# Performance work log

Hardware: AMD Instinct MI355X
Metric: run time of the kernel (lower is better)

The kernel has to match this reference:

```python
import jax, jax.numpy as jnp
import numpy as np

IN_DIM = 1024
OUT_DIM = 128
N = 8192


def setup_inputs() -> dict:
    key = jax.random.key(0)
    ks = jax.random.split(key, 7)
    s = 1.0 / np.sqrt(IN_DIM)
    return {
        "z": jax.random.normal(ks[0], (N, IN_DIM), dtype=jnp.float32),
        "Wq": jax.random.normal(ks[1], (IN_DIM, OUT_DIM), dtype=jnp.float32) * s,
        "bq": jax.random.normal(ks[2], (OUT_DIM,), dtype=jnp.float32) * 0.01,
        "Wk": jax.random.normal(ks[3], (IN_DIM, OUT_DIM), dtype=jnp.float32) * s,
        "bk": jax.random.normal(ks[4], (OUT_DIM,), dtype=jnp.float32) * 0.01,
        "Wv": jax.random.normal(ks[5], (IN_DIM, OUT_DIM), dtype=jnp.float32) * s,
        "bv": jax.random.normal(ks[6], (OUT_DIM,), dtype=jnp.float32) * 0.01,
    }


def reference(z, Wq, bq, Wk, bk, Wv, bv):
    # QKV projections: [N, in_dim] @ [in_dim, out_dim] + bias -> [N, out_dim]
    q = z @ Wq + bq
    k = z @ Wk + bk
    v = z @ Wv + bv
    dh = q.shape[-1]
    # Scores [N, N], scaled by sqrt(dh); softmax over last axis (torch 2-D default)
    scores = (q @ k.T) * (1.0 / jnp.sqrt(jnp.asarray(dh, q.dtype)))
    A = jax.nn.softmax(scores, axis=-1)
    return A @ v
```

## Files before the change

kernel.cpp:

```cpp
#include <hip/hip_runtime.h>


#define N_TOK   8192
#define D_IN    1024
#define D_HEAD  128
#define QSCALE  (0.08838834764831845f * 1.4426950408889634f)
#define SPLIT   8
#define QB      128
#define KVB     64
#define NIT     ((N_TOK / SPLIT) / KVB)

typedef _Float16 half8 __attribute__((ext_vector_type(8)));
typedef _Float16 half4 __attribute__((ext_vector_type(4)));
typedef float f32x4 __attribute__((ext_vector_type(4)));

__global__ void prep_wt(const float* __restrict__ Wq, const float* __restrict__ Wk,
                        const float* __restrict__ Wv, _Float16* __restrict__ Wt) {
    __shared__ float T[32][129];
    const int mat = blockIdx.y;
    const int k0 = blockIdx.x * 32;
    const int t = threadIdx.x;
    const float* W = (mat == 0) ? Wq : (mat == 1) ? Wk : Wv;

    const int krow = t >> 3, nc0 = (t & 7) * 16;
#pragma unroll
    for (int i = 0; i < 4; i++) {
        float4 f = reinterpret_cast<const float4*>(
            W + (size_t)(k0 + krow) * D_HEAD + nc0)[i];
        T[krow][nc0 + i * 4 + 0] = f.x;
        T[krow][nc0 + i * 4 + 1] = f.y;
        T[krow][nc0 + i * 4 + 2] = f.z;
        T[krow][nc0 + i * 4 + 3] = f.w;
    }
    __syncthreads();

    const int n = t >> 1, kh = (t & 1) * 16;
    half8 h0, h1;
#pragma unroll
    for (int j = 0; j < 8; j++) {
        float v0 = T[kh + j][n];
        float v1 = T[kh + 8 + j][n];
        if (mat == 0) { v0 *= QSCALE; v1 *= QSCALE; }
        h0[j] = (_Float16)v0;
        h1[j] = (_Float16)v1;
    }
    _Float16* dst = Wt + (size_t)mat * 131072 + (size_t)n * D_IN + k0 + kh;
    reinterpret_cast<half8*>(dst)[0] = h0;
    reinterpret_cast<half8*>(dst)[1] = h1;
}

__launch_bounds__(256)
__global__ void qkv_gemm(const float* __restrict__ z, const _Float16* __restrict__ Wt,
                         const float* __restrict__ bq, const float* __restrict__ bk,
                         const float* __restrict__ bv,
                         _Float16* __restrict__ Qs, _Float16* __restrict__ Kh,
                         _Float16* __restrict__ Vt) {
    __shared__ __align__(16) char lds[32768];
    char* Ab = lds;
    char* Bb = lds + 16384;

    const int mat = blockIdx.y;
    const int m0 = blockIdx.x * 128;
    const int t = threadIdx.x;
    const int lane = t & 63, w = t >> 6;
    const int l15 = lane & 15, g = lane >> 4;
    const int wm = w >> 1, wn = w & 1;
    const _Float16* Wm = Wt + (size_t)mat * 131072;

    const int srow = t >> 1, sh = t & 1;
    int aw[4], bw[4];
#pragma unroll
    for (int i = 0; i < 4; i++) {
        int u = ((sh * 4 + i) ^ (srow & 7)) << 4;
        aw[i] = srow * 128 + u;
        bw[i] = srow * 128 + u;
    }
    int ru[2];
#pragma unroll
    for (int ct = 0; ct < 2; ct++) ru[ct] = ((ct * 4 + g) ^ (l15 & 7)) << 4;

    f32x4 acc[4][4] = {};

    const float4* zg = reinterpret_cast<const float4*>(
        z + (size_t)(m0 + srow) * D_IN + sh * 32);
    const half8* wg = reinterpret_cast<const half8*>(
        Wm + (size_t)srow * D_IN + sh * 32);

    float4 af[8];
    half8 bf[4];
#pragma unroll
    for (int i = 0; i < 8; i++) af[i] = zg[i];
#pragma unroll
    for (int i = 0; i < 4; i++) bf[i] = wg[i];

    for (int it = 0; it < 16; ++it) {
        __syncthreads();
#pragma unroll
        for (int j = 0; j < 4; j++) {
            half8 h;
            float4 lo = af[2 * j], hi = af[2 * j + 1];
            h[0]=(_Float16)lo.x; h[1]=(_Float16)lo.y; h[2]=(_Float16)lo.z; h[3]=(_Float16)lo.w;
            h[4]=(_Float16)hi.x; h[5]=(_Float16)hi.y; h[6]=(_Float16)hi.z; h[7]=(_Float16)hi.w;
            *reinterpret_cast<half8*>(Ab + aw[j]) = h;
            *reinterpret_cast<half8*>(Bb + bw[j]) = bf[j];
        }
        __syncthreads();

        if (it < 15) {
            zg += 16;
            wg += 8;
#pragma unroll
            for (int i = 0; i < 8; i++) af[i] = zg[i];
#pragma unroll
            for (int i = 0; i < 4; i++) bf[i] = wg[i];
        }

        __builtin_amdgcn_s_setprio(1);
#pragma unroll
        for (int ct = 0; ct < 2; ct++) {
            half8 afr[4], bfr[4];
#pragma unroll
            for (int m16 = 0; m16 < 4; m16++)
                afr[m16] = *reinterpret_cast<half8*>(
                    Ab + (wm * 64 + m16 * 16 + l15) * 128 + ru[ct]);
#pragma unroll
            for (int n16 = 0; n16 < 4; n16++)
                bfr[n16] = *reinterpret_cast<half8*>(
                    Bb + (wn * 64 + n16 * 16 + l15) * 128 + ru[ct]);
#pragma unroll
            for (int m16 = 0; m16 < 4; m16++)
#pragma unroll
                for (int n16 = 0; n16 < 4; n16++)
                    acc[m16][n16] = __builtin_amdgcn_mfma_f32_16x16x32_f16(
                        afr[m16], bfr[n16], acc[m16][n16], 0, 0, 0);
        }
        __builtin_amdgcn_s_setprio(0);
    }

    const float* bias = (mat == 0) ? bq : (mat == 1) ? bk : bv;
    if (mat < 2) {
        _Float16* dst = (mat == 0) ? Qs : Kh;
#pragma unroll
        for (int n16 = 0; n16 < 4; n16++) {
            int n = wn * 64 + n16 * 16 + l15;
            float b = bias[n];
            if (mat == 0) b *= QSCALE;
#pragma unroll
            for (int m16 = 0; m16 < 4; m16++)
#pragma unroll
                for (int r = 0; r < 4; r++) {
                    int m = m0 + wm * 64 + m16 * 16 + g * 4 + r;
                    dst[(size_t)m * D_HEAD + n] = (_Float16)(acc[m16][n16][r] + b);
                }
        }
    } else {
#pragma unroll
        for (int n16 = 0; n16 < 4; n16++) {
            int n = wn * 64 + n16 * 16 + l15;
            float b = bias[n];
#pragma unroll
            for (int m16 = 0; m16 < 4; m16++) {
                half4 pk;
#pragma unroll
                for (int r = 0; r < 4; r++) pk[r] = (_Float16)(acc[m16][n16][r] + b);
                int m = m0 + wm * 64 + m16 * 16 + g * 4;
                *reinterpret_cast<half4*>(&Vt[(size_t)n * N_TOK + m]) = pk;
            }
        }
    }
}

__launch_bounds__(256, 2)
__global__ void attn(const _Float16* __restrict__ Qs, const _Float16* __restrict__ Kh,
                     const _Float16* __restrict__ Vt,
                     _Float16* __restrict__ Opart, float* __restrict__ lpart) {
    __shared__ __align__(16) char lds[49152];
    char* Kb = lds;
    char* Vb = lds + 16384;
    char* Pb = lds + 32768;

    const int t = threadIdx.x;
    const int lane = t & 63, w = t >> 6;
    const int l15 = lane & 15, g = lane >> 4;
    const int q0 = blockIdx.x * QB;
    const int sp = blockIdx.y;
    const int kvA = sp * (N_TOK / SPLIT);

    half8 qa[2][4];
#pragma unroll
    for (int r16 = 0; r16 < 2; r16++)
#pragma unroll
        for (int ct = 0; ct < 4; ct++)
            qa[r16][ct] = *reinterpret_cast<const half8*>(
                Qs + (size_t)(q0 + w * 32 + r16 * 16 + l15) * D_HEAD + ct * 32 + g * 8);

    const int krow = t >> 2, kseg = t & 3;
    const int vd = t >> 1, vh = t & 1;
    int kw[4], vw[4];
#pragma unroll
    for (int i = 0; i < 4; i++) {
        kw[i] = krow * 256 + (((kseg * 4 + i) ^ (krow & 7)) << 4);
        vw[i] = vd * 128 + (((vh * 4 + i) ^ (vd & 7)) << 4);
    }
    int kru[4], vru[2];
#pragma unroll
    for (int ct = 0; ct < 4; ct++) kru[ct] = ((ct * 4 + g) ^ (l15 & 7)) << 4;
#pragma unroll
    for (int s2 = 0; s2 < 2; s2++) vru[s2] = ((s2 * 4 + g) ^ (l15 & 7)) << 4;
    char* Pw = Pb + w * 4096;
    const int phi = l15 >> 3, plo = (l15 & 7) * 2;
    int px[4];
#pragma unroll
    for (int r = 0; r < 4; r++) px[r] = (g * 4 + r) & 7;

    f32x4 o[2][8] = {};
    float lsum[2][4] = {};

    const _Float16* kg = Kh + (size_t)(kvA + krow) * D_HEAD + kseg * 32;
    const _Float16* vg = Vt + (size_t)vd * N_TOK + kvA + vh * 32;
    half8 kr[4], vr[4];
#pragma unroll
    for (int i = 0; i < 4; i++) {
        kr[i] = reinterpret_cast<const half8*>(kg)[i];
        vr[i] = reinterpret_cast<const half8*>(vg)[i];
    }

    for (int it = 0; it < NIT; ++it) {
        __syncthreads();
#pragma unroll
        for (int i = 0; i < 4; i++) {
            *reinterpret_cast<half8*>(Kb + kw[i]) = kr[i];
            *reinterpret_cast<half8*>(Vb + vw[i]) = vr[i];
        }
        __syncthreads();

        if (it + 1 < NIT) {
            kg += (size_t)KVB * D_HEAD;
            vg += KVB;
#pragma unroll
            for (int i = 0; i < 4; i++) {
                kr[i] = reinterpret_cast<const half8*>(kg)[i];
                vr[i] = reinterpret_cast<const half8*>(vg)[i];
            }
        }

        f32x4 sf[2][4] = {};
        __builtin_amdgcn_s_setprio(1);
#pragma unroll
        for (int kt = 0; kt < 4; kt++) {
#pragma unroll
            for (int ct = 0; ct < 4; ct++) {
                half8 kf = *reinterpret_cast<half8*>(Kb + kt * 4096 + l15 * 256 + kru[ct]);
#pragma unroll
                for (int r16 = 0; r16 < 2; r16++)
                    sf[r16][kt] = __builtin_amdgcn_mfma_f32_16x16x32_f16(
                        qa[r16][ct], kf, sf[r16][kt], 0, 0, 0);
            }
        }
        __builtin_amdgcn_s_setprio(0);

#pragma unroll
        for (int r16 = 0; r16 < 2; r16++)
#pragma unroll
            for (int kt = 0; kt < 4; kt++)
#pragma unroll
                for (int r = 0; r < 4; r++) {
                    float p = __builtin_amdgcn_exp2f(sf[r16][kt][r]);
                    lsum[r16][r] += p;
                    *reinterpret_cast<_Float16*>(
                        Pw + r16 * 2048 + (g * 4 + r) * 128 +
                        (((kt * 2 + phi) ^ px[r]) << 4) + plo) = (_Float16)p;
                }

        __builtin_amdgcn_s_setprio(1);
#pragma unroll
        for (int s2 = 0; s2 < 2; s2++) {
            half8 pa[2];
#pragma unroll
            for (int r16 = 0; r16 < 2; r16++)
                pa[r16] = *reinterpret_cast<half8*>(Pw + r16 * 2048 + l15 * 128 + vru[s2]);
#pragma unroll
            for (int dt = 0; dt < 8; dt++) {
                half8 vf = *reinterpret_cast<half8*>(Vb + dt * 2048 + l15 * 128 + vru[s2]);
#pragma unroll
                for (int r16 = 0; r16 < 2; r16++)
                    o[r16][dt] = __builtin_amdgcn_mfma_f32_16x16x32_f16(
                        pa[r16], vf, o[r16][dt], 0, 0, 0);
            }
        }
        __builtin_amdgcn_s_setprio(0);
    }

#pragma unroll
    for (int r16 = 0; r16 < 2; r16++)
#pragma unroll
        for (int r = 0; r < 4; r++) {
            float v = lsum[r16][r];
            v += __shfl_xor(v, 1, 64);
            v += __shfl_xor(v, 2, 64);
            v += __shfl_xor(v, 4, 64);
            v += __shfl_xor(v, 8, 64);
            lsum[r16][r] = v;
        }

    _Float16* Op = Opart + (size_t)sp * N_TOK * D_HEAD;
#pragma unroll
    for (int r16 = 0; r16 < 2; r16++)
#pragma unroll
        for (int dt = 0; dt < 8; dt++)
#pragma unroll
            for (int r = 0; r < 4; r++)
                Op[(size_t)(q0 + w * 32 + r16 * 16 + g * 4 + r) * D_HEAD + dt * 16 + l15] =
                    (_Float16)o[r16][dt][r];
    if (l15 == 0) {
#pragma unroll
        for (int r16 = 0; r16 < 2; r16++)
#pragma unroll
            for (int r = 0; r < 4; r++)
                lpart[sp * N_TOK + q0 + w * 32 + r16 * 16 + g * 4 + r] = lsum[r16][r];
    }
}

__global__ void combine(const _Float16* __restrict__ Opart, const float* __restrict__ lpart,
                        float* __restrict__ out) {
    int i = blockIdx.x * 256 + threadIdx.x;
    int base = i * 8;
    int m = base >> 7;
    float acc[8] = {};
    float den = 0.f;
#pragma unroll
    for (int s = 0; s < SPLIT; s++) {
        half8 h = *reinterpret_cast<const half8*>(
            Opart + (size_t)s * N_TOK * D_HEAD + base);
#pragma unroll
        for (int j = 0; j < 8; j++) acc[j] += (float)h[j];
        den += lpart[s * N_TOK + m];
    }
    float inv = 1.f / den;
    float4 o0, o1;
    o0.x = acc[0]*inv; o0.y = acc[1]*inv; o0.z = acc[2]*inv; o0.w = acc[3]*inv;
    o1.x = acc[4]*inv; o1.y = acc[5]*inv; o1.z = acc[6]*inv; o1.w = acc[7]*inv;
    reinterpret_cast<float4*>(out + base)[0] = o0;
    reinterpret_cast<float4*>(out + base)[1] = o1;
}

extern "C" void kernel_launch(void* const* d_in, const int* in_sizes, int n_in,
                              void* d_out, int out_size, void* d_ws, size_t ws_size,
                              hipStream_t stream) {
    const float* z  = (const float*)d_in[0];
    const float* Wq = (const float*)d_in[1];
    const float* bq = (const float*)d_in[2];
    const float* Wk = (const float*)d_in[3];
    const float* bk = (const float*)d_in[4];
    const float* Wv = (const float*)d_in[5];
    const float* bv = (const float*)d_in[6];
    float* out = (float*)d_out;

    char* ws = (char*)d_ws;
    _Float16* Wt = (_Float16*)(ws);
    _Float16* Qs = (_Float16*)(ws + 786432);
    _Float16* Kh = (_Float16*)(ws + 786432 + 2097152);
    _Float16* Vt = (_Float16*)(ws + 786432 + 2 * 2097152);
    _Float16* Opart = (_Float16*)(ws + 786432 + 3 * 2097152);
    float* lpart = (float*)(ws + 786432 + 3 * 2097152 +
                            (size_t)SPLIT * N_TOK * D_HEAD * 2);

    prep_wt<<<dim3(32, 3), 256, 0, stream>>>(Wq, Wk, Wv, Wt);
    qkv_gemm<<<dim3(64, 3), 256, 0, stream>>>(z, Wt, bq, bk, bv, Qs, Kh, Vt);
    attn<<<dim3(N_TOK / QB, SPLIT), 256, 0, stream>>>(Qs, Kh, Vt, Opart, lpart);
    combine<<<512, 256, 0, stream>>>(Opart, lpart, out);
}
```

Measured before the change: 159.7 us.

## Double-buffer K/V in LDS and pass P through registers via shuffles

```diff
diff --git a/kernel.cpp b/kernel.cpp
--- a/kernel.cpp
+++ b/kernel.cpp
@@ -13,6 +13,13 @@
 typedef _Float16 half8 __attribute__((ext_vector_type(8)));
 typedef _Float16 half4 __attribute__((ext_vector_type(4)));
 typedef float f32x4 __attribute__((ext_vector_type(4)));
+
+static __device__ __forceinline__ int pkrtz(float a, float b) {
+    auto h = __builtin_amdgcn_cvt_pkrtz(a, b);
+    return __builtin_bit_cast(int, h);
+}
+
+union I4H8 { int i[4]; half8 h; };
 
 __global__ void prep_wt(const float* __restrict__ Wq, const float* __restrict__ Wk,
                         const float* __restrict__ Wv, _Float16* __restrict__ Wt) {
@@ -174,10 +181,7 @@
 __global__ void attn(const _Float16* __restrict__ Qs, const _Float16* __restrict__ Kh,
                      const _Float16* __restrict__ Vt,
                      _Float16* __restrict__ Opart, float* __restrict__ lpart) {
-    __shared__ __align__(16) char lds[49152];
-    char* Kb = lds;
-    char* Vb = lds + 16384;
-    char* Pb = lds + 32768;
+    __shared__ __align__(16) char lds[65536];
 
     const int t = threadIdx.x;
     const int lane = t & 63, w = t >> 6;
@@ -188,11 +192,11 @@
 
     half8 qa[2][4];
 #pragma unroll
-    for (int r16 = 0; r16 < 2; r16++)
+    for (int qg = 0; qg < 2; qg++)
 #pragma unroll
         for (int ct = 0; ct < 4; ct++)
-            qa[r16][ct] = *reinterpret_cast<const half8*>(
-                Qs + (size_t)(q0 + w * 32 + r16 * 16 + l15) * D_HEAD + ct * 32 + g * 8);
+            qa[qg][ct] = *reinterpret_cast<const half8*>(
+                Qs + (size_t)(q0 + w * 32 + qg * 16 + l15) * D_HEAD + ct * 32 + g * 8);
 
     const int krow = t >> 2, kseg = t & 3;
     const int vd = t >> 1, vh = t & 1;
@@ -206,15 +210,14 @@
 #pragma unroll
     for (int ct = 0; ct < 4; ct++) kru[ct] = ((ct * 4 + g) ^ (l15 & 7)) << 4;
 #pragma unroll
-    for (int s2 = 0; s2 < 2; s2++) vru[s2] = ((s2 * 4 + g) ^ (l15 & 7)) << 4;
-    char* Pw = Pb + w * 4096;
-    const int phi = l15 >> 3, plo = (l15 & 7) * 2;
-    int px[4];
-#pragma unroll
-    for (int r = 0; r < 4; r++) px[r] = (g * 4 + r) & 7;
+    for (int ks = 0; ks < 2; ks++) vru[ks] = ((ks * 4 + g) ^ (l15 & 7)) << 4;
+
+    const int s0 = l15 + 32 * (g & 1);
+    const int s1 = s0 + 16;
+    const bool hi_t = (g & 2) != 0;
 
     f32x4 o[2][8] = {};
-    float lsum[2][4] = {};
+    float lsum[2] = {0.f, 0.f};
 
     const _Float16* kg = Kh + (size_t)(kvA + krow) * D_HEAD + kseg * 32;
     const _Float16* vg = Vt + (size_t)vd * N_TOK + kvA + vh * 32;
@@ -224,17 +227,49 @@
         kr[i] = reinterpret_cast<const half8*>(kg)[i];
         vr[i] = reinterpret_cast<const half8*>(vg)[i];
     }
+#pragma unroll
+    for (int i = 0; i < 4; i++) {
+        *reinterpret_cast<half8*>(lds + kw[i])         = kr[i];
+        *reinterpret_cast<half8*>(lds + 16384 + vw[i]) = vr[i];
+    }
+    kg += (size_t)KVB * D_HEAD;
+    vg += KVB;
+#pragma unroll
+    for (int i = 0; i < 4; i++) {
+        kr[i] = reinterpret_cast<const half8*>(kg)[i];
+        vr[i] = reinterpret_cast<const half8*>(vg)[i];
+    }
+    __syncthreads();
 
     for (int it = 0; it < NIT; ++it) {
-        __syncthreads();
-#pragma unroll
-        for (int i = 0; i < 4; i++) {
-            *reinterpret_cast<half8*>(Kb + kw[i]) = kr[i];
-            *reinterpret_cast<half8*>(Vb + vw[i]) = vr[i];
-        }
-        __syncthreads();
+        char* Kb = lds + (it & 1) * 32768;
+        char* Vb = Kb + 16384;
+        char* Kn = lds + ((it & 1) ^ 1) * 32768;
+        char* Vn = Kn + 16384;
+
+        f32x4 sf[2][4] = {};
+        __builtin_amdgcn_s_setprio(1);
+#pragma unroll
+        for (int kt = 0; kt < 4; kt++) {
+#pragma unroll
+            for (int ct = 0; ct < 4; ct++) {
+                half8 kf = *reinterpret_cast<half8*>(Kb + kt * 4096 + l15 * 256 + kru[ct]);
+#pragma unroll
+                for (int qg = 0; qg < 2; qg++)
+                    sf[qg][kt] = __builtin_amdgcn_mfma_f32_16x16x32_f16(
+                        kf, qa[qg][ct], sf[qg][kt], 0, 0, 0);
+            }
+        }
+        __builtin_amdgcn_s_setprio(0);
 
         if (it + 1 < NIT) {
+#pragma unroll
+            for (int i = 0; i < 4; i++) {
+                *reinterpret_cast<half8*>(Kn + kw[i]) = kr[i];
+                *reinterpret_cast<half8*>(Vn + vw[i]) = vr[i];
+            }
+        }
+        if (it + 2 < NIT) {
             kg += (size_t)KVB * D_HEAD;
             vg += KVB;
 #pragma unroll
@@ -244,80 +279,79 @@
             }
         }
 
-        f32x4 sf[2][4] = {};
+        int pk[2][4][2];
+#pragma unroll
+        for (int qg = 0; qg < 2; qg++)
+#pragma unroll
+            for (int kt = 0; kt < 4; kt++) {
+                float e0 = __builtin_amdgcn_exp2f(sf[qg][kt][0]);
+                float e1 = __builtin_amdgcn_exp2f(sf[qg][kt][1]);
+                float e2 = __builtin_amdgcn_exp2f(sf[qg][kt][2]);
+                float e3 = __builtin_amdgcn_exp2f(sf[qg][kt][3]);
+                lsum[qg] += (e0 + e1) + (e2 + e3);
+                pk[qg][kt][0] = pkrtz(e0, e1);
+                pk[qg][kt][1] = pkrtz(e2, e3);
+            }
+
         __builtin_amdgcn_s_setprio(1);
 #pragma unroll
-        for (int kt = 0; kt < 4; kt++) {
-#pragma unroll
-            for (int ct = 0; ct < 4; ct++) {
-                half8 kf = *reinterpret_cast<half8*>(Kb + kt * 4096 + l15 * 256 + kru[ct]);
-#pragma unroll
-                for (int r16 = 0; r16 < 2; r16++)
-                    sf[r16][kt] = __builtin_amdgcn_mfma_f32_16x16x32_f16(
-                        qa[r16][ct], kf, sf[r16][kt], 0, 0, 0);
+        for (int ks = 0; ks < 2; ks++) {
+            half8 pa[2];
+#pragma unroll
+            for (int qg = 0; qg < 2; qg++) {
+                int a0 = __shfl(pk[qg][2 * ks][0],     s0);
+                int b0 = __shfl(pk[qg][2 * ks + 1][0], s0);
+                int a1 = __shfl(pk[qg][2 * ks][1],     s0);
+                int b1 = __shfl(pk[qg][2 * ks + 1][1], s0);
+                int a2 = __shfl(pk[qg][2 * ks][0],     s1);
+                int b2 = __shfl(pk[qg][2 * ks + 1][0], s1);
+                int a3 = __shfl(pk[qg][2 * ks][1],     s1);
+                int b3 = __shfl(pk[qg][2 * ks + 1][1], s1);
+                I4H8 u;
+                u.i[0] = hi_t ? b0 : a0;
+                u.i[1] = hi_t ? b1 : a1;
+                u.i[2] = hi_t ? b2 : a2;
+                u.i[3] = hi_t ? b3 : a3;
+                pa[qg] = u.h;
+            }
+#pragma unroll
+            for (int dt = 0; dt < 8; dt++) {
+                half8 vf = *reinterpret_cast<half8*>(Vb + dt * 2048 + l15 * 128 + vru[ks]);
+#pragma unroll
+                for (int qg = 0; qg < 2; qg++)
+                    o[qg][dt] = __builtin_amdgcn_mfma_f32_16x16x32_f16(
+                        vf, pa[qg], o[qg][dt], 0, 0, 0);
             }
         }
         __builtin_amdgcn_s_setprio(0);
 
-#pragma unroll
-        for (int r16 = 0; r16 < 2; r16++)
-#pragma unroll
-            for (int kt = 0; kt < 4; kt++)
-#pragma unroll
-                for (int r = 0; r < 4; r++) {
-                    float p = __builtin_amdgcn_exp2f(sf[r16][kt][r]);
-                    lsum[r16][r] += p;
-                    *reinterpret_cast<_Float16*>(
-                        Pw + r16 * 2048 + (g * 4 + r) * 128 +
-                        (((kt * 2 + phi) ^ px[r]) << 4) + plo) = (_Float16)p;
-                }
-
-        __builtin_amdgcn_s_setprio(1);
-#pragma unroll
-        for (int s2 = 0; s2 < 2; s2++) {
-            half8 pa[2];
-#pragma unroll
-            for (int r16 = 0; r16 < 2; r16++)
-                pa[r16] = *reinterpret_cast<half8*>(Pw + r16 * 2048 + l15 * 128 + vru[s2]);
-#pragma unroll
-            for (int dt = 0; dt < 8; dt++) {
-                half8 vf = *reinterpret_cast<half8*>(Vb + dt * 2048 + l15 * 128 + vru[s2]);
-#pragma unroll
-                for (int r16 = 0; r16 < 2; r16++)
-                    o[r16][dt] = __builtin_amdgcn_mfma_f32_16x16x32_f16(
-                        pa[r16], vf, o[r16][dt], 0, 0, 0);
-            }
-        }
-        __builtin_amdgcn_s_setprio(0);
-    }
-
-#pragma unroll
-    for (int r16 = 0; r16 < 2; r16++)
-#pragma unroll
-        for (int r = 0; r < 4; r++) {
-            float v = lsum[r16][r];
-            v += __shfl_xor(v, 1, 64);
-            v += __shfl_xor(v, 2, 64);
-            v += __shfl_xor(v, 4, 64);
-            v += __shfl_xor(v, 8, 64);
-            lsum[r16][r] = v;
-        }
+        __syncthreads();
+    }
+
+#pragma unroll
+    for (int qg = 0; qg < 2; qg++) {
+        float v = lsum[qg];
+        v += __shfl_xor(v, 16, 64);
+        v += __shfl_xor(v, 32, 64);
+        lsum[qg] = v;
+    }
 
     _Float16* Op = Opart + (size_t)sp * N_TOK * D_HEAD;
 #pragma unroll
-    for (int r16 = 0; r16 < 2; r16++)
-#pragma unroll
-        for (int dt = 0; dt < 8; dt++)
-#pragma unroll
-            for (int r = 0; r < 4; r++)
-                Op[(size_t)(q0 + w * 32 + r16 * 16 + g * 4 + r) * D_HEAD + dt * 16 + l15] =
-                    (_Float16)o[r16][dt][r];
-    if (l15 == 0) {
-#pragma unroll
-        for (int r16 = 0; r16 < 2; r16++)
-#pragma unroll
-            for (int r = 0; r < 4; r++)
-                lpart[sp * N_TOK + q0 + w * 32 + r16 * 16 + g * 4 + r] = lsum[r16][r];
+    for (int qg = 0; qg < 2; qg++) {
+        const size_t qrow = (size_t)(q0 + w * 32 + qg * 16 + l15) * D_HEAD;
+#pragma unroll
+        for (int dt = 0; dt < 8; dt++) {
+            int2 pv;
+            pv.x = pkrtz(o[qg][dt][0], o[qg][dt][1]);
+            pv.y = pkrtz(o[qg][dt][2], o[qg][dt][3]);
+            *reinterpret_cast<int2*>(Op + qrow + dt * 16 + g * 4) = pv;
+        }
+    }
+    if (lane < 16) {
+#pragma unroll
+        for (int qg = 0; qg < 2; qg++)
+            lpart[sp * N_TOK + q0 + w * 32 + qg * 16 + l15] = lsum[qg];
     }
 }
 
```

Result: no change. 160.0 us (+0.2%).
